# Optimization experiments

Hardware: AMD Instinct MI355X
Metric: run time of the kernel (lower is better)

## Reference

```python
import jax, jax.numpy as jnp
import numpy as np

NUM_LEVELS = 8
CODEBOOK_SIZE = 1024
D_MODEL = 512


def setup_inputs() -> dict:
    key = jax.random.key(0)
    kx, kc = jax.random.split(key)
    x = jax.random.normal(kx, (8, 4096, D_MODEL), dtype=jnp.float32)
    # stacked embedding tables, one per RVQ level: [L, K, D]
    codebooks = jax.random.normal(kc, (NUM_LEVELS, CODEBOOK_SIZE, D_MODEL), dtype=jnp.float32)
    return {"x": x, "codebooks": codebooks}


def reference(x, codebooks):
    """Residual VQ: per level, nearest-codebook lookup on the residual.

    x: [B, N, D], codebooks: [L, K, D].
    Returns (quantized [B, N, D] with straight-through estimator, indices [B, N, L]).
    """
    residual = x
    q_sum = jnp.zeros_like(x)
    all_indices = []
    for l in range(codebooks.shape[0]):
        cb = codebooks[l]  # [K, D]
        # squared Euclidean distance; argmin matches torch.cdist argmin
        r2 = jnp.sum(residual * residual, axis=-1, keepdims=True)      # [B, N, 1]
        c2 = jnp.sum(cb * cb, axis=-1)                                  # [K]
        cross = jnp.einsum("bnd,kd->bnk", residual, cb)                # [B, N, K]
        dist2 = r2 - 2.0 * cross + c2                                   # [B, N, K]
        idx = jnp.argmin(dist2, axis=-1)                                # [B, N]
        all_indices.append(idx)
        q = cb[idx]                                                     # gather: [B, N, D]
        q_sum = q_sum + q
        residual = residual - q
    # straight-through: forward value is q_sum, gradient flows to x only
    quantized = x + jax.lax.stop_gradient(q_sum - x)
    return quantized, jnp.stack(all_indices, axis=-1)
```

## Files before the change

### kernel.cpp

```cpp
#include <hip/hip_runtime.h>
#include <stdint.h>

#define NLV 8
#define KCB 1024
#define DM  512
#define NTOK (8*4096)
#define BETA 0.00390625f

typedef _Float16 f16;
typedef f16  f16x4 __attribute__((ext_vector_type(4)));
typedef f16  f16x8 __attribute__((ext_vector_type(8)));
typedef float f32x4 __attribute__((ext_vector_type(4)));

typedef __attribute__((address_space(1))) const unsigned int* as1p;
typedef __attribute__((address_space(3))) unsigned int*       as3p;
__device__ __forceinline__ void gll16(const void* g, void* l) {
    __builtin_amdgcn_global_load_lds((as1p)g, (as3p)l, 16, 0, 0);
}

__global__ void c2_kernel(const float* __restrict__ cbs, float* __restrict__ c2) {
    int row  = blockIdx.x;
    int lane = threadIdx.x;
    const float4* p4 = (const float4*)(cbs + (size_t)row * DM);
    float4 a = p4[lane];
    float4 b = p4[lane + 64];
    float s = a.x*a.x + a.y*a.y + a.z*a.z + a.w*a.w
            + b.x*b.x + b.y*b.y + b.z*b.z + b.w*b.w;
    float t = (float)(f16)a.x + (float)(f16)a.y + (float)(f16)a.z + (float)(f16)a.w
            + (float)(f16)b.x + (float)(f16)b.y + (float)(f16)b.z + (float)(f16)b.w;
    #pragma unroll
    for (int off = 32; off > 0; off >>= 1) {
        s += __shfl_down(s, off, 64);
        t += __shfl_down(t, off, 64);
    }
    if (lane == 0) c2[row] = s + 2.0f * BETA * t;
}

__global__ void split_kernel(const float* __restrict__ src,
                             f16* __restrict__ hi, f16* __restrict__ lo) {
    size_t i = (size_t)blockIdx.x * 256 + threadIdx.x;
    float4 v = ((const float4*)src)[i];
    f16x4 h, l;
    h.x = (f16)v.x; l.x = (f16)((v.x - (float)h.x) + BETA);
    h.y = (f16)v.y; l.y = (f16)((v.y - (float)h.y) + BETA);
    h.z = (f16)v.z; l.z = (f16)((v.z - (float)h.z) + BETA);
    h.w = (f16)v.w; l.w = (f16)((v.w - (float)h.w) + BETA);
    ((f16x4*)hi)[i] = h;
    ((f16x4*)lo)[i] = l;
}

#define MBT  64
#define NCH  256
#define KS   32
#define NTHR 256
#define BUFB 40960

__global__ __launch_bounds__(NTHR, 2)
void rvq_mfma(const float* __restrict__ xin, float* __restrict__ qout,
              const float* __restrict__ cbs,
              const f16* __restrict__ Bhi, const f16* __restrict__ Blo,
              f16* __restrict__ Ahi, f16* __restrict__ Alo,
              const float* __restrict__ c2g, float* __restrict__ idxout,
              int lvl, int is_last)
{
    __shared__ char smem[2 * BUFB];
    const int tid  = threadIdx.x;
    const int lane = tid & 63;
    const int wn   = tid >> 6;
    const int tx   = lane & 15;
    const int q    = lane >> 4;
    const size_t tok0 = (size_t)blockIdx.x * MBT;

    const f16*   Bh_l = Bhi + (size_t)lvl * KCB * DM;
    const f16*   Bl_l = Blo + (size_t)lvl * KCB * DM;
    const float* c2l  = c2g + lvl * KCB;
    const float* cbl  = cbs + (size_t)lvl * KCB * DM;

    const int srow = tid >> 2;
    const int sg   = (tid & 3) ^ ((srow >> 1) & 3);
    const int rsw  = q ^ ((tx >> 1) & 3);

    auto stage = [&](char* buf, int cb0, int k0) {
        const int ko = k0 + sg * 8;
        char* wb = buf + wn * 1024;
        const size_t ga = (tok0 + srow) * (size_t)DM + ko;
        gll16(&Ahi[ga], wb);
        gll16(&Alo[ga], wb + 4096);
        #pragma unroll
        for (int i = 0; i < 4; ++i) {
            const size_t gb = (size_t)(cb0 + 64 * i + srow) * DM + ko;
            gll16(&Bh_l[gb], wb +  8192 + 4096 * i);
            gll16(&Bl_l[gb], wb + 24576 + 4096 * i);
        }
    };

    int aoff[4], boff[4];
    #pragma unroll
    for (int i = 0; i < 4; ++i) aoff[i] = (i * 16 + tx) * 64 + rsw * 16;
    #pragma unroll
    for (int j = 0; j < 4; ++j) boff[j] = (wn * 64 + j * 16 + tx) * 64 + rsw * 16;

    float bestv[16];
    int   besti[16];
    #pragma unroll
    for (int t = 0; t < 16; ++t) { bestv[t] = 3.4e38f; besti[t] = 0; }

    stage(smem, 0, 0);

    for (int ch = 0; ch < KCB / NCH; ++ch) {
        f32x4 acc[4][4];
        #pragma unroll
        for (int i = 0; i < 4; ++i)
            #pragma unroll
            for (int j = 0; j < 4; ++j) acc[i][j] = (f32x4)0.0f;

        for (int kk = 0; kk < 16; ++kk) {
            const int gk = ch * 16 + kk;
            char* bb = smem + (gk & 1) * BUFB;
            char* bn = smem + ((gk & 1) ^ 1) * BUFB;
            __syncthreads();
            if (gk + 1 < 64)
                stage(bn, ((gk + 1) >> 4) * NCH, ((gk + 1) & 15) * KS);

            f16x8 ah[4], al[4], bh[4], bl[4];
            #pragma unroll
            for (int i = 0; i < 4; ++i) {
                ah[i] = *(const f16x8*)(bb +        aoff[i]);
                al[i] = *(const f16x8*)(bb + 4096 + aoff[i]);
            }
            #pragma unroll
            for (int j = 0; j < 4; ++j) {
                bh[j] = *(const f16x8*)(bb +  8192 + boff[j]);
                bl[j] = *(const f16x8*)(bb + 24576 + boff[j]);
            }
            #pragma unroll
            for (int j = 0; j < 4; ++j)
                #pragma unroll
                for (int i = 0; i < 4; ++i)
                    acc[i][j] = __builtin_amdgcn_mfma_f32_16x16x32_f16(ah[i], bh[j], acc[i][j], 0, 0, 0);
            #pragma unroll
            for (int j = 0; j < 4; ++j)
                #pragma unroll
                for (int i = 0; i < 4; ++i)
                    acc[i][j] = __builtin_amdgcn_mfma_f32_16x16x32_f16(ah[i], bl[j], acc[i][j], 0, 0, 0);
            #pragma unroll
            for (int j = 0; j < 4; ++j)
                #pragma unroll
                for (int i = 0; i < 4; ++i)
                    acc[i][j] = __builtin_amdgcn_mfma_f32_16x16x32_f16(al[i], bh[j], acc[i][j], 0, 0, 0);
        }

        const int cb0 = ch * NCH;
        #pragma unroll
        for (int j = 0; j < 4; ++j) {
            int n = cb0 + wn * 64 + j * 16 + tx;
            float c2v = c2l[n];
            #pragma unroll
            for (int i = 0; i < 4; ++i)
                #pragma unroll
                for (int r = 0; r < 4; ++r) {
                    float s = fmaf(-2.f, acc[i][j][r], c2v);
                    int t = i * 4 + r;
                    if (s < bestv[t]) { bestv[t] = s; besti[t] = n; }
                }
        }
    }

    #pragma unroll
    for (int t = 0; t < 16; ++t) {
        float v = bestv[t]; int bi = besti[t];
        #pragma unroll
        for (int off = 1; off < 16; off <<= 1) {
            float ov = __shfl_xor(v, off, 64);
            int   oi = __shfl_xor(bi, off, 64);
            if (ov < v || (ov == v && oi < bi)) { v = ov; bi = oi; }
        }
        bestv[t] = v; besti[t] = bi;
    }

    float* redV = (float*)smem;
    int*   redI = (int*)(smem + 1024);
    int*   kbst = (int*)(smem + 2048);
    __syncthreads();
    if (tx == 0) {
        #pragma unroll
        for (int i = 0; i < 4; ++i)
            #pragma unroll
            for (int r = 0; r < 4; ++r) {
                int m = i * 16 + q * 4 + r;
                redV[wn * 64 + m] = bestv[i * 4 + r];
                redI[wn * 64 + m] = besti[i * 4 + r];
            }
    }
    __syncthreads();
    if (tid < MBT) {
        float bv = redV[tid]; int bi = redI[tid];
        #pragma unroll
        for (int w = 1; w < 4; ++w) {
            float v  = redV[w * 64 + tid];
            int   ii = redI[w * 64 + tid];
            if (v < bv || (v == bv && ii < bi)) { bv = v; bi = ii; }
        }
        kbst[tid] = bi;
        idxout[(tok0 + tid) * NLV + lvl] = (float)bi;
    }
    __syncthreads();

    #pragma unroll 4
    for (int it = 0; it < 16; ++it) {
        int e  = it * NTHR + tid;
        int t  = e >> 6, d8 = e & 63;
        size_t go = (tok0 + t) * (size_t)DM + d8 * 8;
        f16x8 h8 = *(const f16x8*)&Ahi[go];
        f16x8 l8 = *(const f16x8*)&Alo[go];
        const float* cp = &cbl[(size_t)kbst[t] * DM + d8 * 8];
        float4 c0 = *(const float4*)cp;
        float4 c1 = *(const float4*)(cp + 4);
        float r[8];
        r[0] = (float)h8[0] + ((float)l8[0] - BETA) - c0.x;
        r[1] = (float)h8[1] + ((float)l8[1] - BETA) - c0.y;
        r[2] = (float)h8[2] + ((float)l8[2] - BETA) - c0.z;
        r[3] = (float)h8[3] + ((float)l8[3] - BETA) - c0.w;
        r[4] = (float)h8[4] + ((float)l8[4] - BETA) - c1.x;
        r[5] = (float)h8[5] + ((float)l8[5] - BETA) - c1.y;
        r[6] = (float)h8[6] + ((float)l8[6] - BETA) - c1.z;
        r[7] = (float)h8[7] + ((float)l8[7] - BETA) - c1.w;
        if (is_last) {
            float4 x0 = *(const float4*)&xin[go];
            float4 x1 = *(const float4*)&xin[go + 4];
            float4 q0 = make_float4(x0.x - r[0], x0.y - r[1], x0.z - r[2], x0.w - r[3]);
            float4 q1 = make_float4(x1.x - r[4], x1.y - r[5], x1.z - r[6], x1.w - r[7]);
            *(float4*)&qout[go]     = q0;
            *(float4*)&qout[go + 4] = q1;
        } else {
            f16x8 h, l;
            #pragma unroll
            for (int k = 0; k < 8; ++k) {
                h[k] = (f16)r[k];
                l[k] = (f16)((r[k] - (float)h[k]) + BETA);
            }
            *(f16x8*)&Ahi[go] = h;
            *(f16x8*)&Alo[go] = l;
        }
    }
}

extern "C" void kernel_launch(void* const* d_in, const int* in_sizes, int n_in,
                              void* d_out, int out_size, void* d_ws, size_t ws_size,
                              hipStream_t stream) {
    const float* x   = (const float*)d_in[0];
    const float* cbs = (const float*)d_in[1];
    float* qout   = (float*)d_out;
    float* idxout = qout + (size_t)NTOK * DM;

    const size_t B_ELE = (size_t)NLV * KCB * DM;
    const size_t A_ELE = (size_t)NTOK * DM;

    f16* Bhi = (f16*)d_ws;
    f16* Blo = Bhi + B_ELE;
    f16* Ahi = Blo + B_ELE;
    f16* Alo = Ahi + A_ELE;
    float* c2 = (float*)(Alo + A_ELE);

    split_kernel<<<(int)(B_ELE / 4 / 256), 256, 0, stream>>>(cbs, Bhi, Blo);
    split_kernel<<<(int)(A_ELE / 4 / 256), 256, 0, stream>>>(x, Ahi, Alo);
    c2_kernel<<<NLV * KCB, 64, 0, stream>>>(cbs, c2);

    const int nblocks = NTOK / MBT;
    for (int l = 0; l < NLV; ++l) {
        rvq_mfma<<<nblocks, NTHR, 0, stream>>>(x, qout, cbs,
                                               Bhi, Blo, Ahi, Alo, c2, idxout,
                                               l, (l == NLV - 1) ? 1 : 0);
    }
}
```

Before: 1.131 ms.

## Double token tile to 128 with 8 waves sharing codebook tiles; add MFMA setprio

```diff
diff --git a/kernel.cpp b/kernel.cpp
--- a/kernel.cpp
+++ b/kernel.cpp
@@ -49,11 +49,11 @@
     ((f16x4*)lo)[i] = l;
 }
 
-#define MBT  64
+#define MBT  128
 #define NCH  256
 #define KS   32
-#define NTHR 256
-#define BUFB 40960
+#define NTHR 512
+#define BUFB 49152
 
 __global__ __launch_bounds__(NTHR, 2)
 void rvq_mfma(const float* __restrict__ xin, float* __restrict__ qout,
@@ -66,7 +66,9 @@
     __shared__ char smem[2 * BUFB];
     const int tid  = threadIdx.x;
     const int lane = tid & 63;
-    const int wn   = tid >> 6;
+    const int w    = tid >> 6;
+    const int wn   = w & 3;
+    const int wm   = w >> 2;
     const int tx   = lane & 15;
     const int q    = lane >> 4;
     const size_t tok0 = (size_t)blockIdx.x * MBT;
@@ -76,27 +78,28 @@
     const float* c2l  = c2g + lvl * KCB;
     const float* cbl  = cbs + (size_t)lvl * KCB * DM;
 
-    const int srow = tid >> 2;
-    const int sg   = (tid & 3) ^ ((srow >> 1) & 3);
+    const int rloc = lane >> 2;
+    const int sg   = (lane & 3) ^ ((lane >> 3) & 3);
     const int rsw  = q ^ ((tx >> 1) & 3);
 
-    auto stage = [&](char* buf, int cb0, int k0) {
-        const int ko = k0 + sg * 8;
-        char* wb = buf + wn * 1024;
-        const size_t ga = (tok0 + srow) * (size_t)DM + ko;
-        gll16(&Ahi[ga], wb);
-        gll16(&Alo[ga], wb + 4096);
-        #pragma unroll
-        for (int i = 0; i < 4; ++i) {
-            const size_t gb = (size_t)(cb0 + 64 * i + srow) * DM + ko;
-            gll16(&Bh_l[gb], wb +  8192 + 4096 * i);
-            gll16(&Bl_l[gb], wb + 24576 + 4096 * i);
-        }
+    const f16* pAh = Ahi + (tok0 + w * 16 + rloc) * (size_t)DM + sg * 8;
+    const f16* pAl = Alo + (tok0 + w * 16 + rloc) * (size_t)DM + sg * 8;
+    const size_t bRow = (size_t)(w * 16 + rloc) * DM + sg * 8;
+
+    auto stage = [&](char* buf, int gk2) {
+        const int ko    = (gk2 & 15) * KS;
+        const size_t bo = (size_t)((gk2 >> 4) * NCH) * DM + ko;
+        gll16(pAh + ko, buf + w * 1024);
+        gll16(pAl + ko, buf + 8192 + w * 1024);
+        gll16(Bh_l + bo + bRow,            buf + 16384 + w * 1024);
+        gll16(Bh_l + bo + bRow + 128 * DM, buf + 16384 + (w + 8) * 1024);
+        gll16(Bl_l + bo + bRow,            buf + 32768 + w * 1024);
+        gll16(Bl_l + bo + bRow + 128 * DM, buf + 32768 + (w + 8) * 1024);
     };
 
     int aoff[4], boff[4];
     #pragma unroll
-    for (int i = 0; i < 4; ++i) aoff[i] = (i * 16 + tx) * 64 + rsw * 16;
+    for (int i = 0; i < 4; ++i) aoff[i] = (wm * 64 + i * 16 + tx) * 64 + rsw * 16;
     #pragma unroll
     for (int j = 0; j < 4; ++j) boff[j] = (wn * 64 + j * 16 + tx) * 64 + rsw * 16;
 
@@ -105,7 +108,7 @@
     #pragma unroll
     for (int t = 0; t < 16; ++t) { bestv[t] = 3.4e38f; besti[t] = 0; }
 
-    stage(smem, 0, 0);
+    stage(smem, 0);
 
     for (int ch = 0; ch < KCB / NCH; ++ch) {
         f32x4 acc[4][4];
@@ -118,21 +121,24 @@
             const int gk = ch * 16 + kk;
             char* bb = smem + (gk & 1) * BUFB;
             char* bn = smem + ((gk & 1) ^ 1) * BUFB;
+
             __syncthreads();
             if (gk + 1 < 64)
-                stage(bn, ((gk + 1) >> 4) * NCH, ((gk + 1) & 15) * KS);
+                stage(bn, gk + 1);
 
             f16x8 ah[4], al[4], bh[4], bl[4];
             #pragma unroll
             for (int i = 0; i < 4; ++i) {
-                ah[i] = *(const f16x8*)(bb +        aoff[i]);
-                al[i] = *(const f16x8*)(bb + 4096 + aoff[i]);
+                ah[i] = *(const f16x8*)(bb + aoff[i]);
+                al[i] = *(const f16x8*)(bb + 8192 + aoff[i]);
             }
             #pragma unroll
             for (int j = 0; j < 4; ++j) {
-                bh[j] = *(const f16x8*)(bb +  8192 + boff[j]);
-                bl[j] = *(const f16x8*)(bb + 24576 + boff[j]);
-            }
+                bh[j] = *(const f16x8*)(bb + 16384 + boff[j]);
+                bl[j] = *(const f16x8*)(bb + 32768 + boff[j]);
+            }
+
+            __builtin_amdgcn_s_setprio(1);
             #pragma unroll
             for (int j = 0; j < 4; ++j)
                 #pragma unroll
@@ -148,6 +154,7 @@
                 #pragma unroll
                 for (int i = 0; i < 4; ++i)
                     acc[i][j] = __builtin_amdgcn_mfma_f32_16x16x32_f16(al[i], bh[j], acc[i][j], 0, 0, 0);
+            __builtin_amdgcn_s_setprio(0);
         }
 
         const int cb0 = ch * NCH;
@@ -179,26 +186,26 @@
     }
 
     float* redV = (float*)smem;
-    int*   redI = (int*)(smem + 1024);
-    int*   kbst = (int*)(smem + 2048);
+    int*   redI = (int*)(smem + 2048);
+    int*   kbst = (int*)(smem + 4096);
     __syncthreads();
     if (tx == 0) {
         #pragma unroll
         for (int i = 0; i < 4; ++i)
             #pragma unroll
             for (int r = 0; r < 4; ++r) {
-                int m = i * 16 + q * 4 + r;
-                redV[wn * 64 + m] = bestv[i * 4 + r];
-                redI[wn * 64 + m] = besti[i * 4 + r];
+                int m = wm * 64 + i * 16 + q * 4 + r;
+                redV[wn * 128 + m] = bestv[i * 4 + r];
+                redI[wn * 128 + m] = besti[i * 4 + r];
             }
     }
     __syncthreads();
     if (tid < MBT) {
         float bv = redV[tid]; int bi = redI[tid];
         #pragma unroll
-        for (int w = 1; w < 4; ++w) {
-            float v  = redV[w * 64 + tid];
-            int   ii = redI[w * 64 + tid];
+        for (int ww = 1; ww < 4; ++ww) {
+            float v  = redV[ww * 128 + tid];
+            int   ii = redI[ww * 128 + tid];
             if (v < bv || (v == bv && ii < bi)) { bv = v; bi = ii; }
         }
         kbst[tid] = bi;
```

After: 1.128 ms, median of 3. Within noise of the previous version (-0.3%).
